# Optimization experiments

Measured on AMD Instinct MI355X. Metric: run time of the kernel, lower is better.

Reference implementation:

```python
import jax, jax.numpy as jnp
import numpy as np

H = 16        # num_heads
BUCKET = 64   # bucket_size == chunk length
NEG = -1e9


def setup_inputs() -> dict:
    key0 = jax.random.key(0)
    ks = jax.random.split(key0, 12)
    B, S, DM = 2, 4096, 1024
    R, NB = 4, S // BUCKET  # num_hashes, n_buckets = 64
    dk = DM // H
    n = lambda k, shp: jax.random.normal(k, shp, dtype=jnp.float32)
    w = lambda k, shp: 0.02 * jax.random.normal(k, shp, dtype=jnp.float32)
    return {
        "query": n(ks[0], (B, S, DM)),
        "key": n(ks[1], (B, S, DM)),
        "value": n(ks[2], (B, S, DM)),
        "Wq": w(ks[3], (DM, DM)), "bq": w(ks[4], (DM,)),
        "Wk": w(ks[5], (DM, DM)), "bk": w(ks[6], (DM,)),
        "Wv": w(ks[7], (DM, DM)), "bv": w(ks[8], (DM,)),
        "Wo": w(ks[9], (DM, DM)), "bo": w(ks[10], (DM,)),
        "rotations": n(ks[11], (R, dk, NB // 2)),
    }


def reference(query, key, value, Wq, bq, Wk, bk, Wv, bv, Wo, bo, rotations):
    B, S, dm = query.shape
    dk = Wq.shape[0] // H
    R = rotations.shape[0]

    def proj(x, W, b):  # -> [B,H,S,dk]
        return (x @ W.T + b).reshape(B, S, H, dk).transpose(0, 2, 1, 3)

    q = proj(query, Wq, bq)
    k = proj(key, Wk, bk)
    v = proj(value, Wv, bv)

    # --- LSH bucketing: bucket = argmax([xR, -xR]) per hash round ---
    rq = jnp.einsum('bhsd,rdn->rbhsn', q, rotations)
    rk = jnp.einsum('bhsd,rdn->rbhsn', k, rotations)
    qbuck = jnp.argmax(jnp.concatenate([rq, -rq], axis=-1), axis=-1)  # [R,B,H,S]
    kbuck = jnp.argmax(jnp.concatenate([rk, -rk], axis=-1), axis=-1)

    # --- stable sort tokens by bucket (tie-break by position) ---
    pos = jnp.arange(S)
    q_idx = jnp.argsort(qbuck * S + pos, axis=-1)  # [R,B,H,S]
    k_idx = jnp.argsort(kbuck * S + pos, axis=-1)

    def gather(x, idx):  # x [B,H,S,dk] -> [R,B,H,S,dk]
        xb = jnp.broadcast_to(x, (R,) + x.shape)
        return jnp.take_along_axis(xb, idx[..., None], axis=3)

    qs = gather(q, q_idx)
    ks_ = gather(k, k_idx)
    vs = gather(v, k_idx)
    qb_s = jnp.take_along_axis(qbuck, q_idx, axis=-1)
    kb_s = jnp.take_along_axis(kbuck, k_idx, axis=-1)

    # --- chunk; each query chunk attends to its own + previous key chunk ---
    nc = S // BUCKET
    qs = qs.reshape(R, B, H, nc, BUCKET, dk)
    ks_ = ks_.reshape(R, B, H, nc, BUCKET, dk)
    vs = vs.reshape(R, B, H, nc, BUCKET, dk)
    qb_c = qb_s.reshape(R, B, H, nc, BUCKET)
    kb_c = kb_s.reshape(R, B, H, nc, BUCKET)

    k_ext = jnp.concatenate([jnp.roll(ks_, 1, axis=3), ks_], axis=4)   # [R,B,H,nc,2C,dk]
    v_ext = jnp.concatenate([jnp.roll(vs, 1, axis=3), vs], axis=4)
    kb_ext = jnp.concatenate([jnp.roll(kb_c, 1, axis=3), kb_c], axis=4)

    scores = jnp.einsum('rbhncd,rbhnkd->rbhnck', qs, k_ext) / jnp.sqrt(jnp.float32(dk))
    same_bucket = qb_c[..., :, None] == kb_ext[..., None, :]           # [R,B,H,nc,C,2C]
    scores = jnp.where(same_bucket, scores, NEG)
    attn = jax.nn.softmax(scores, axis=-1)
    out = jnp.einsum('rbhnck,rbhnkd->rbhncd', attn, v_ext).reshape(R, B, H, S, dk)

    # --- unsort back to original positions, average hash rounds ---
    inv = jnp.argsort(q_idx, axis=-1)
    out = jnp.take_along_axis(out, inv[..., None], axis=3)
    out = out.mean(axis=0)                                             # [B,H,S,dk]
    out = out.transpose(0, 2, 1, 3).reshape(B, S, H * dk)
    return out @ Wo.T + bo
```

## Files before the change

### kernel.cpp

```cpp
#include <hip/hip_runtime.h>
#include <hip/hip_bf16.h>
#include <math.h>

#define BB 2
#define SS 4096
#define DMM 1024
#define HH 16
#define DKK 64
#define RR 4
#define NROT 32
#define NC 64

template<int MODE>
__global__ __launch_bounds__(256)
void gemm_xwt(const float* __restrict__ A, const float* __restrict__ W,
              const float* __restrict__ bias, float* __restrict__ dst, int mode)
{
    #pragma clang fp contract(off)
    __shared__ __align__(16) float AsT[16][68];
    __shared__ __align__(16) float WsT[16][68];
    const int K = DMM;
    const int t = threadIdx.x;
    const int bx = blockIdx.x, by = blockIdx.y;
    const int tx = t & 15, ty = t >> 4;
    const int i0 = ty * 4, j0 = tx * 4;
    const int rl = t >> 2, kq = (t & 3) * 4;
    const float* Ap = A + ((size_t)(by * 64 + rl)) * K + kq;
    const float* Wp = W + ((size_t)(bx * 64 + rl)) * K + kq;
    float acc0[4][4] = {}, acc1[4][4] = {};
    for (int k0 = 0; k0 < K; k0 += 16) {
        const float4 av = *(const float4*)(Ap + k0);
        const float4 wv = *(const float4*)(Wp + k0);
        __syncthreads();
        AsT[kq+0][rl] = av.x; AsT[kq+1][rl] = av.y; AsT[kq+2][rl] = av.z; AsT[kq+3][rl] = av.w;
        WsT[kq+0][rl] = wv.x; WsT[kq+1][rl] = wv.y; WsT[kq+2][rl] = wv.z; WsT[kq+3][rl] = wv.w;
        __syncthreads();
        float (*ac)[4] = (MODE == 1 && k0 >= 512) ? acc1 : acc0;
        #pragma unroll
        for (int kk = 0; kk < 16; kk++) {
            const float4 a = *(const float4*)&AsT[kk][i0];
            const float4 w = *(const float4*)&WsT[kk][j0];
            const float a_[4] = {a.x, a.y, a.z, a.w};
            const float w_[4] = {w.x, w.y, w.z, w.w};
            #pragma unroll
            for (int ii = 0; ii < 4; ii++)
                #pragma unroll
                for (int jj = 0; jj < 4; jj++)
                    ac[ii][jj] = __builtin_fmaf(a_[ii], w_[jj], ac[ii][jj]);
        }
    }
    float cf[4][4];
    #pragma unroll
    for (int ii = 0; ii < 4; ii++)
        #pragma unroll
        for (int jj = 0; jj < 4; jj++)
            cf[ii][jj] = (MODE == 1) ? (acc0[ii][jj] + acc1[ii][jj]) : acc0[ii][jj];
    const float4 bv = *(const float4*)(bias + bx * 64 + j0);
    const int m0 = by * 64 + i0;
    if (mode == 0) {
        const int h = bx;
        #pragma unroll
        for (int ii = 0; ii < 4; ii++) {
            const int m = m0 + ii, b = m >> 12, s = m & (SS - 1);
            const float4 o = make_float4(cf[ii][0]+bv.x, cf[ii][1]+bv.y,
                                         cf[ii][2]+bv.z, cf[ii][3]+bv.w);
            *(float4*)(dst + (((size_t)b * HH + h) * SS + s) * DKK + j0) = o;
        }
    } else {
        #pragma unroll
        for (int ii = 0; ii < 4; ii++) {
            const float4 o = make_float4(cf[ii][0]+bv.x, cf[ii][1]+bv.y,
                                         cf[ii][2]+bv.z, cf[ii][3]+bv.w);
            *(float4*)(dst + (size_t)(m0 + ii) * DMM + bx * 64 + j0) = o;
        }
    }
}

__global__ __launch_bounds__(256)
void bucketize(const float* __restrict__ x, const float* __restrict__ rot,
               int* __restrict__ buck)
{
    #pragma clang fp contract(off)
    const int r = blockIdx.z, bh = blockIdx.y;
    const int s = blockIdx.x * 256 + threadIdx.x;
    const float* rp = rot + (size_t)r * DKK * NROT;
    const float* xp = x + ((size_t)bh * SS + s) * DKK;
    float qv[DKK];
    #pragma unroll
    for (int d = 0; d < DKK; d += 4) {
        const float4 v = *(const float4*)(xp + d);
        qv[d] = v.x; qv[d+1] = v.y; qv[d+2] = v.z; qv[d+3] = v.w;
    }
    float rq[NROT];
    #pragma unroll
    for (int n = 0; n < NROT; n++) rq[n] = 0.f;
    for (int d = 0; d < DKK; d++) {
        const float qd = qv[d];
        const float4* rv4 = (const float4*)(rp + d * NROT);
        #pragma unroll
        for (int n4 = 0; n4 < 8; n4++) {
            const float4 rv = rv4[n4];
            const float p0 = qd * rv.x;
            const float p1 = qd * rv.y;
            const float p2 = qd * rv.z;
            const float p3 = qd * rv.w;
            rq[n4*4+0] = rq[n4*4+0] + p0;
            rq[n4*4+1] = rq[n4*4+1] + p1;
            rq[n4*4+2] = rq[n4*4+2] + p2;
            rq[n4*4+3] = rq[n4*4+3] + p3;
        }
    }
    float best = rq[0]; int bi = 0;
    #pragma unroll
    for (int n = 1; n < NROT; n++) if (rq[n] > best) { best = rq[n]; bi = n; }
    #pragma unroll
    for (int n = 0; n < NROT; n++) { const float v = -rq[n]; if (v > best) { best = v; bi = NROT + n; } }
    buck[((size_t)r * BB * HH + bh) * SS + s] = bi;
}

__global__ __launch_bounds__(64)
void bucket_sort(const int* __restrict__ buck, int* __restrict__ idx)
{
    const int seg = blockIdx.x;
    const int* bp = buck + (size_t)seg * SS;
    int* ip = idx + (size_t)seg * SS;
    __shared__ int hist[64][65];
    const int c = threadIdx.x;
    for (int j = 0; j < 64; j++) hist[c][j] = 0;
    __syncthreads();
    for (int e = 0; e < 64; e++) hist[c][bp[c * 64 + e]]++;
    __syncthreads();
    int run = 0;
    for (int cc = 0; cc < 64; cc++) { const int tv = hist[cc][c]; hist[cc][c] = run; run += tv; }
    int x = run;
    for (int off = 1; off < 64; off <<= 1) { const int v = __shfl_up(x, off); if (c >= off) x += v; }
    const int base = x - run;
    for (int cc = 0; cc < 64; cc++) hist[cc][c] += base;
    __syncthreads();
    for (int e = 0; e < 64; e++) {
        const int s = c * 64 + e;
        const int bk = bp[s];
        ip[hist[c][bk]++] = s;
    }
}

__global__ __launch_bounds__(256)
void lsh_attn(const float* __restrict__ qg, const float* __restrict__ kg,
              const float* __restrict__ vg, const int* __restrict__ qbuck,
              const int* __restrict__ kbuck, const int* __restrict__ qidx,
              const int* __restrict__ kidx, float* __restrict__ oacc)
{
    const int n = blockIdx.x, bh = blockIdx.y, r = blockIdx.z;
    const int b = bh >> 4, h = bh & 15;
    const size_t seg = ((size_t)r * BB * HH + bh) * SS;
    const float* qbase = qg + (size_t)bh * SS * DKK;
    const float* kbase = kg + (size_t)bh * SS * DKK;
    const float* vbase = vg + (size_t)bh * SS * DKK;

    __shared__ __align__(16) float qs[64][68];
    __shared__ __align__(16) float ke[128][68];
    __shared__ __align__(16) float ve[128][68];
    __shared__ __align__(16) float ps[64][132];
    __shared__ int qbv[64], kbv[128], qsrc[64];

    const int t = threadIdx.x;
    {
        const int row = t >> 2, q4 = (t & 3) * 16;
        const int sq = qidx[seg + n * 64 + row];
        if ((t & 3) == 0) { qsrc[row] = sq; qbv[row] = qbuck[seg + sq]; }
        const float* src = qbase + (size_t)sq * DKK + q4;
        #pragma unroll
        for (int x = 0; x < 16; x += 4)
            *(float4*)&qs[row][q4 + x] = *(const float4*)(src + x);
    }
    #pragma unroll
    for (int pass = 0; pass < 2; pass++) {
        const int row = pass * 64 + (t >> 2), q4 = (t & 3) * 16;
        const int cn = (pass == 0) ? ((n + NC - 1) & (NC - 1)) : n;
        const int sk = kidx[seg + cn * 64 + (row & 63)];
        if ((t & 3) == 0) kbv[row] = kbuck[seg + sk];
        const float* ksrc = kbase + (size_t)sk * DKK + q4;
        const float* vsrc = vbase + (size_t)sk * DKK + q4;
        #pragma unroll
        for (int x = 0; x < 16; x += 4) {
            *(float4*)&ke[row][q4 + x] = *(const float4*)(ksrc + x);
            *(float4*)&ve[row][q4 + x] = *(const float4*)(vsrc + x);
        }
    }
    __syncthreads();

    const int ig = t >> 3, jg = t & 7;
    const int r0 = ig * 2;
    float sc0[16], sc1[16];
    #pragma unroll
    for (int jj = 0; jj < 16; jj++) { sc0[jj] = 0.f; sc1[jj] = 0.f; }
    #pragma unroll
    for (int d4 = 0; d4 < DKK; d4 += 4) {
        const float4 a0 = *(const float4*)&qs[r0][d4];
        const float4 a1 = *(const float4*)&qs[r0 + 1][d4];
        #pragma unroll
        for (int jj = 0; jj < 16; jj++) {
            const float4 kv = *(const float4*)&ke[jj * 8 + jg][d4];
            sc0[jj] += a0.x*kv.x + a0.y*kv.y + a0.z*kv.z + a0.w*kv.w;
            sc1[jj] += a1.x*kv.x + a1.y*kv.y + a1.z*kv.z + a1.w*kv.w;
        }
    }
    const int qb0 = qbv[r0], qb1 = qbv[r0 + 1];
    float m0 = -INFINITY, m1 = -INFINITY;
    #pragma unroll
    for (int jj = 0; jj < 16; jj++) {
        const int kb = kbv[jj * 8 + jg];
        float s0 = sc0[jj] * 0.125f; if (kb != qb0) s0 = -1e9f;
        float s1 = sc1[jj] * 0.125f; if (kb != qb1) s1 = -1e9f;
        sc0[jj] = s0; sc1[jj] = s1;
        m0 = fmaxf(m0, s0); m1 = fmaxf(m1, s1);
    }
    m0 = fmaxf(m0, __shfl_xor(m0, 1)); m1 = fmaxf(m1, __shfl_xor(m1, 1));
    m0 = fmaxf(m0, __shfl_xor(m0, 2)); m1 = fmaxf(m1, __shfl_xor(m1, 2));
    m0 = fmaxf(m0, __shfl_xor(m0, 4)); m1 = fmaxf(m1, __shfl_xor(m1, 4));
    float sum0 = 0.f, sum1 = 0.f;
    #pragma unroll
    for (int jj = 0; jj < 16; jj++) {
        const float e0 = __expf(sc0[jj] - m0);
        const float e1 = __expf(sc1[jj] - m1);
        sc0[jj] = e0; sc1[jj] = e1;
        sum0 += e0; sum1 += e1;
    }
    sum0 += __shfl_xor(sum0, 1); sum1 += __shfl_xor(sum1, 1);
    sum0 += __shfl_xor(sum0, 2); sum1 += __shfl_xor(sum1, 2);
    sum0 += __shfl_xor(sum0, 4); sum1 += __shfl_xor(sum1, 4);
    const float inv0 = 1.f / sum0, inv1 = 1.f / sum1;
    #pragma unroll
    for (int jj = 0; jj < 16; jj++) {
        const int j = jj * 8 + jg;
        ps[r0][j]     = sc0[jj] * inv0;
        ps[r0 + 1][j] = sc1[jj] * inv1;
    }
    __syncthreads();

    const int dg = t & 7;
    float a0[8] = {0,0,0,0,0,0,0,0}, a1[8] = {0,0,0,0,0,0,0,0};
    #pragma unroll
    for (int jb = 0; jb < 32; jb++) {
        const float4 p0 = *(const float4*)&ps[r0][jb * 4];
        const float4 p1 = *(const float4*)&ps[r0 + 1][jb * 4];
        const float pj0[4] = {p0.x, p0.y, p0.z, p0.w};
        const float pj1[4] = {p1.x, p1.y, p1.z, p1.w};
        #pragma unroll
        for (int jx = 0; jx < 4; jx++) {
            const int j = jb * 4 + jx;
            const float4 v0 = *(const float4*)&ve[j][dg * 8];
            const float4 v1 = *(const float4*)&ve[j][dg * 8 + 4];
            a0[0] += pj0[jx]*v0.x; a0[1] += pj0[jx]*v0.y; a0[2] += pj0[jx]*v0.z; a0[3] += pj0[jx]*v0.w;
            a0[4] += pj0[jx]*v1.x; a0[5] += pj0[jx]*v1.y; a0[6] += pj0[jx]*v1.z; a0[7] += pj0[jx]*v1.w;
            a1[0] += pj1[jx]*v0.x; a1[1] += pj1[jx]*v0.y; a1[2] += pj1[jx]*v0.z; a1[3] += pj1[jx]*v0.w;
            a1[4] += pj1[jx]*v1.x; a1[5] += pj1[jx]*v1.y; a1[6] += pj1[jx]*v1.z; a1[7] += pj1[jx]*v1.w;
        }
    }
    {
        const int s0_ = qsrc[r0], s1_ = qsrc[r0 + 1];
        float* d0 = oacc + ((size_t)b * SS + s0_) * DMM + h * DKK + dg * 8;
        float* d1 = oacc + ((size_t)b * SS + s1_) * DMM + h * DKK + dg * 8;
        #pragma unroll
        for (int x = 0; x < 8; x++) {
            atomicAdd(d0 + x, a0[x] * 0.25f);
            atomicAdd(d1 + x, a1[x] * 0.25f);
        }
    }
}

extern "C" void kernel_launch(void* const* d_in, const int* in_sizes, int n_in,
                              void* d_out, int out_size, void* d_ws, size_t ws_size,
                              hipStream_t stream) {
    const float* query = (const float*)d_in[0];
    const float* key   = (const float*)d_in[1];
    const float* value = (const float*)d_in[2];
    const float* Wq = (const float*)d_in[3];
    const float* bq = (const float*)d_in[4];
    const float* Wk = (const float*)d_in[5];
    const float* bk = (const float*)d_in[6];
    const float* Wv = (const float*)d_in[7];
    const float* bv = (const float*)d_in[8];
    const float* Wo = (const float*)d_in[9];
    const float* bo = (const float*)d_in[10];
    const float* rot = (const float*)d_in[11];
    float* out = (float*)d_out;

    const size_t PROJ = (size_t)BB * HH * SS * DKK;
    const size_t OACC = (size_t)BB * SS * DMM;
    const size_t BKN  = (size_t)RR * BB * HH * SS;

    float* qp   = (float*)d_ws;
    float* kp   = qp + PROJ;
    float* vp   = kp + PROJ;
    float* oacc = vp + PROJ;
    int* qbk = (int*)(oacc + OACC);
    int* kbk = qbk + BKN;
    int* qix = kbk + BKN;
    int* kix = qix + BKN;

    hipMemsetAsync(oacc, 0, OACC * sizeof(float), stream);

    dim3 gg(DMM / 64, (BB * SS) / 64);
    gemm_xwt<1><<<gg, 256, 0, stream>>>(query, Wq, bq, qp, 0);
    gemm_xwt<1><<<gg, 256, 0, stream>>>(key,   Wk, bk, kp, 0);
    gemm_xwt<0><<<gg, 256, 0, stream>>>(value, Wv, bv, vp, 0);

    dim3 gb(SS / 256, BB * HH, RR);
    bucketize<<<gb, 256, 0, stream>>>(qp, rot, qbk);
    bucketize<<<gb, 256, 0, stream>>>(kp, rot, kbk);

    bucket_sort<<<RR * BB * HH, 64, 0, stream>>>(qbk, qix);
    bucket_sort<<<RR * BB * HH, 64, 0, stream>>>(kbk, kix);

    dim3 ga(NC, BB * HH, RR);
    lsh_attn<<<ga, 256, 0, stream>>>(qp, kp, vp, qbk, kbk, qix, kix, oacc);

    gemm_xwt<0><<<gg, 256, 0, stream>>>(oacc, Wo, bo, out, 1);
}
```

Measured before the change: 2.908 ms.

## Share one LDS buffer for K and V and pass probabilities via shuffles

```diff
diff --git a/kernel.cpp b/kernel.cpp
--- a/kernel.cpp
+++ b/kernel.cpp
@@ -158,10 +158,8 @@
     const float* vbase = vg + (size_t)bh * SS * DKK;
 
     __shared__ __align__(16) float qs[64][68];
-    __shared__ __align__(16) float ke[128][68];
-    __shared__ __align__(16) float ve[128][68];
-    __shared__ __align__(16) float ps[64][132];
-    __shared__ int qbv[64], kbv[128], qsrc[64];
+    __shared__ __align__(16) float kv[128][68];
+    __shared__ int qbv[64], kbv[128], qsrc[64], ksrc[128];
 
     const int t = threadIdx.x;
     {
@@ -178,14 +176,11 @@
         const int row = pass * 64 + (t >> 2), q4 = (t & 3) * 16;
         const int cn = (pass == 0) ? ((n + NC - 1) & (NC - 1)) : n;
         const int sk = kidx[seg + cn * 64 + (row & 63)];
-        if ((t & 3) == 0) kbv[row] = kbuck[seg + sk];
-        const float* ksrc = kbase + (size_t)sk * DKK + q4;
-        const float* vsrc = vbase + (size_t)sk * DKK + q4;
-        #pragma unroll
-        for (int x = 0; x < 16; x += 4) {
-            *(float4*)&ke[row][q4 + x] = *(const float4*)(ksrc + x);
-            *(float4*)&ve[row][q4 + x] = *(const float4*)(vsrc + x);
-        }
+        if ((t & 3) == 0) { kbv[row] = kbuck[seg + sk]; ksrc[row] = sk; }
+        const float* src = kbase + (size_t)sk * DKK + q4;
+        #pragma unroll
+        for (int x = 0; x < 16; x += 4)
+            *(float4*)&kv[row][q4 + x] = *(const float4*)(src + x);
     }
     __syncthreads();
 
@@ -200,9 +195,9 @@
         const float4 a1 = *(const float4*)&qs[r0 + 1][d4];
         #pragma unroll
         for (int jj = 0; jj < 16; jj++) {
-            const float4 kv = *(const float4*)&ke[jj * 8 + jg][d4];
-            sc0[jj] += a0.x*kv.x + a0.y*kv.y + a0.z*kv.z + a0.w*kv.w;
-            sc1[jj] += a1.x*kv.x + a1.y*kv.y + a1.z*kv.z + a1.w*kv.w;
+            const float4 kvv = *(const float4*)&kv[jj * 8 + jg][d4];
+            sc0[jj] += a0.x*kvv.x + a0.y*kvv.y + a0.z*kvv.z + a0.w*kvv.w;
+            sc1[jj] += a1.x*kvv.x + a1.y*kvv.y + a1.z*kvv.z + a1.w*kvv.w;
         }
     }
     const int qb0 = qbv[r0], qb1 = qbv[r0 + 1];
@@ -231,30 +226,38 @@
     sum0 += __shfl_xor(sum0, 4); sum1 += __shfl_xor(sum1, 4);
     const float inv0 = 1.f / sum0, inv1 = 1.f / sum1;
     #pragma unroll
-    for (int jj = 0; jj < 16; jj++) {
-        const int j = jj * 8 + jg;
-        ps[r0][j]     = sc0[jj] * inv0;
-        ps[r0 + 1][j] = sc1[jj] * inv1;
-    }
-    __syncthreads();
-
-    const int dg = t & 7;
+    for (int jj = 0; jj < 16; jj++) { sc0[jj] *= inv0; sc1[jj] *= inv1; }
+
+    __syncthreads();
+    #pragma unroll
+    for (int pass = 0; pass < 2; pass++) {
+        const int row = pass * 64 + (t >> 2), q4 = (t & 3) * 16;
+        const int sk = ksrc[row];
+        const float* src = vbase + (size_t)sk * DKK + q4;
+        #pragma unroll
+        for (int x = 0; x < 16; x += 4)
+            *(float4*)&kv[row][q4 + x] = *(const float4*)(src + x);
+    }
+    __syncthreads();
+
+    const int dg = jg;
+    const int laneBase = (t & 63) & ~7;
     float a0[8] = {0,0,0,0,0,0,0,0}, a1[8] = {0,0,0,0,0,0,0,0};
     #pragma unroll
-    for (int jb = 0; jb < 32; jb++) {
-        const float4 p0 = *(const float4*)&ps[r0][jb * 4];
-        const float4 p1 = *(const float4*)&ps[r0 + 1][jb * 4];
-        const float pj0[4] = {p0.x, p0.y, p0.z, p0.w};
-        const float pj1[4] = {p1.x, p1.y, p1.z, p1.w};
-        #pragma unroll
-        for (int jx = 0; jx < 4; jx++) {
-            const int j = jb * 4 + jx;
-            const float4 v0 = *(const float4*)&ve[j][dg * 8];
-            const float4 v1 = *(const float4*)&ve[j][dg * 8 + 4];
-            a0[0] += pj0[jx]*v0.x; a0[1] += pj0[jx]*v0.y; a0[2] += pj0[jx]*v0.z; a0[3] += pj0[jx]*v0.w;
-            a0[4] += pj0[jx]*v1.x; a0[5] += pj0[jx]*v1.y; a0[6] += pj0[jx]*v1.z; a0[7] += pj0[jx]*v1.w;
-            a1[0] += pj1[jx]*v0.x; a1[1] += pj1[jx]*v0.y; a1[2] += pj1[jx]*v0.z; a1[3] += pj1[jx]*v0.w;
-            a1[4] += pj1[jx]*v1.x; a1[5] += pj1[jx]*v1.y; a1[6] += pj1[jx]*v1.z; a1[7] += pj1[jx]*v1.w;
+    for (int s = 0; s < 8; s++) {
+        const int jsrc = (jg + s) & 7;
+        const int srcLane = laneBase | jsrc;
+        #pragma unroll
+        for (int jj = 0; jj < 16; jj++) {
+            const float p0 = __shfl(sc0[jj], srcLane);
+            const float p1 = __shfl(sc1[jj], srcLane);
+            const int j = jj * 8 + jsrc;
+            const float4 v0 = *(const float4*)&kv[j][dg * 8];
+            const float4 v1 = *(const float4*)&kv[j][dg * 8 + 4];
+            a0[0] += p0*v0.x; a0[1] += p0*v0.y; a0[2] += p0*v0.z; a0[3] += p0*v0.w;
+            a0[4] += p0*v1.x; a0[5] += p0*v1.y; a0[6] += p0*v1.z; a0[7] += p0*v1.w;
+            a1[0] += p1*v0.x; a1[1] += p1*v0.y; a1[2] += p1*v0.z; a1[3] += p1*v0.w;
+            a1[4] += p1*v1.x; a1[5] += p1*v1.y; a1[6] += p1*v1.z; a1[7] += p1*v1.w;
         }
     }
     {
```

Result: faster. 2.512 ms (-13.6%).
